# Performance work log

Measured on AMD Instinct MI355X. Metric: run time of the kernel, lower is better.

The kernel has to match this reference:

```python
import jax, jax.numpy as jnp
import numpy as np

NUM_CLASSES = 1000
N, C = 8192, 256

def setup_inputs() -> dict:
    key = jax.random.key(0)
    k1, k2, k3 = jax.random.split(key, 3)
    p = jax.random.normal(k1, (N, C), dtype=jnp.float32)
    z = jax.random.normal(k2, (N, C), dtype=jnp.float32)
    t = jax.random.uniform(k3, (N, NUM_CLASSES), dtype=jnp.float32, minval=1e-4, maxval=1.0)
    targets = t / jnp.sum(t, axis=1, keepdims=True)  # valid soft-label distribution
    return {"p": p, "z": z, "targets": targets}

def reference(p, z, targets):
    z = jax.lax.stop_gradient(z)  # z.detach()
    # F.normalize(dim=1), eps=1e-12
    p = p / jnp.maximum(jnp.linalg.norm(p, axis=1, keepdims=True), 1e-12)
    zn = z / jnp.maximum(jnp.linalg.norm(z, axis=1, keepdims=True), 1e-12)
    dot_product = -jnp.matmul(p, zn.T)  # [N, N]
    # entropy of soft targets, NaN rows (any exact-zero entry) zeroed
    prod = targets * jnp.log(targets)
    entr = -jnp.sum(prod, axis=1)
    entr = jnp.where(jnp.isnan(entr), 0.0, entr)
    norm_entr = entr / jnp.log(jnp.float32(NUM_CLASSES))
    r = 1.0 - norm_entr
    mask1 = jnp.outer(r, r)  # [N, N]
    # cosine similarity Gram of targets (torch cosine_similarity eps=1e-8)
    tnorm = jnp.linalg.norm(targets, axis=1)
    denom = jnp.maximum(tnorm[:, None] * tnorm[None, :], 1e-8)
    mask2 = jnp.matmul(targets, targets.T) / denom  # [N, N]
    n = dot_product.shape[0]
    mask_anchor_out = 1.0 - jnp.eye(n, dtype=dot_product.dtype)
    mask_combined = mask1 * mask2 * mask_anchor_out
    sel = dot_product * mask_combined
    # mean over nonzero entries (jit-safe: sum / count of nonzeros)
    nz = (sel != 0.0)
    return jnp.sum(sel) / jnp.sum(nz).astype(sel.dtype)
```

## Files before the change

### kernel.cpp

```cpp
#include <hip/hip_runtime.h>
#include <math.h>

#define NROWS 8192
#define CDIM 256
#define KDIM 1000
#define KPAD 1024

#define BC 128
#define BK 64
#define BI 8

typedef __attribute__((ext_vector_type(8))) short bf16x8;
typedef __attribute__((ext_vector_type(4))) float f32x4;
typedef _Float16 f16;
typedef __attribute__((ext_vector_type(4))) _Float16 f16x4;

__device__ __forceinline__ unsigned short f2bf(float x) {
  unsigned int u = __float_as_uint(x);
  u += 0x7fffu + ((u >> 16) & 1u);
  return (unsigned short)(u >> 16);
}
__device__ __forceinline__ float bf2f(unsigned short h) {
  return __uint_as_float(((unsigned int)h) << 16);
}

__device__ __forceinline__ void gl16(const void* g, void* l) {
  __builtin_amdgcn_global_load_lds(
      (const __attribute__((address_space(1))) unsigned int*)g,
      (__attribute__((address_space(3))) unsigned int*)l, 16, 0, 0);
}

__global__ __launch_bounds__(256, 4) void prep_kernel(
    const float* __restrict__ p, const float* __restrict__ z,
    const float* __restrict__ t,
    unsigned short* __restrict__ gAhi, unsigned short* __restrict__ gAlo,
    unsigned short* __restrict__ gBhi, unsigned short* __restrict__ gBlo,
    unsigned short* __restrict__ gUhi, unsigned short* __restrict__ gUlo,
    float* __restrict__ diag) {
  __shared__ float tbuf[8 * 1028];
  __shared__ float st_s[8], uu_s[8], sa_s[8], sb_s[8];
  __shared__ double r_s[8];
  const int tid = threadIdx.x;
  const int w = tid >> 6, lane = tid & 63;
  const int stripe = blockIdx.x;
  const int istep = stripe >> 2;
  const int qtr = stripe & 3;
  const int i0 = stripe * 8;

#pragma unroll
  for (int rr = 0; rr < 2; ++rr) {
    const int row = 2 * w + rr;
    const float* trow = t + (size_t)(i0 + row) * KDIM;
    float stt = 0.f, ent = 0.f, zfl = 0.f;
#pragma unroll
    for (int c = 0; c < 4; ++c) {
      const int k4 = c * 64 + lane;
      float4 v = make_float4(0.f, 0.f, 0.f, 0.f);
      if (k4 < 250) {
        v = *(const float4*)(trow + k4 * 4);
        const float vv[4] = {v.x, v.y, v.z, v.w};
#pragma unroll
        for (int q = 0; q < 4; ++q) {
          stt += vv[q] * vv[q];
          if (vv[q] > 0.f) ent += vv[q] * logf(vv[q]);
          else zfl = 1.f;
        }
      }
      *(float4*)&tbuf[row * 1028 + k4 * 4] = v;
    }
#pragma unroll
    for (int off = 32; off; off >>= 1) {
      stt += __shfl_xor(stt, off);
      ent += __shfl_xor(ent, off);
      zfl += __shfl_xor(zfl, off);
    }
    if (lane == 0) {
      const float tnorm = sqrtf(stt);
      st_s[row] = 1.f / tnorm;
      uu_s[row] = stt / (tnorm * tnorm);
      const float entr = (zfl > 0.f) ? 0.f : (-ent);
      r_s[row] = 1.0 - (double)entr / log(1000.0);
    }
  }
  __syncthreads();

#pragma unroll
  for (int it = 0; it < 4; ++it) {
    const int item = it * 256 + tid;
    const int kt8 = item >> 7;
    const int kf = (item >> 4) & 7;
    const int cl = item & 15;
    const int kcl = kf * 16 + cl;
    unsigned int hi[4], lo[4];
#pragma unroll
    for (int q = 0; q < 4; ++q) {
      const int r0 = 2 * q, r1 = r0 + 1;
      const float v0 = tbuf[r0 * 1028 + kt8 * 128 + kcl] * st_s[r0];
      const float v1 = tbuf[r1 * 1028 + kt8 * 128 + kcl] * st_s[r1];
      const unsigned short h0 = f2bf(v0), h1 = f2bf(v1);
      hi[q] = (unsigned int)h0 | ((unsigned int)h1 << 16);
      const unsigned short e0 = f2bf(v0 - bf2f(h0));
      const unsigned short e1 = f2bf(v1 - bf2f(h1));
      lo[q] = (unsigned int)e0 | ((unsigned int)e1 << 16);
    }
    const size_t off = ((size_t)(kt8 * 256 + istep)) * 8192
                       + (size_t)kf * 1024 + (size_t)(qtr * 16 + cl) * 16;
    *(uint4*)((char*)gUhi + off) = make_uint4(hi[0], hi[1], hi[2], hi[3]);
    *(uint4*)((char*)gUlo + off) = make_uint4(lo[0], lo[1], lo[2], lo[3]);
  }
  __syncthreads();

  float* ptile = tbuf;
  float* ztile = tbuf + 8 * 260;
#pragma unroll
  for (int rr = 0; rr < 2; ++rr) {
    const int row = 2 * w + rr;
    const float* prow = p + (size_t)(i0 + row) * CDIM;
    const float* zrow = z + (size_t)(i0 + row) * CDIM;
    const float4 pv = *(const float4*)(prow + lane * 4);
    const float4 zv = *(const float4*)(zrow + lane * 4);
    *(float4*)&ptile[row * 260 + lane * 4] = pv;
    *(float4*)&ztile[row * 260 + lane * 4] = zv;
    float sp = pv.x * pv.x + pv.y * pv.y + pv.z * pv.z + pv.w * pv.w;
    float sz = zv.x * zv.x + zv.y * zv.y + zv.z * zv.z + zv.w * zv.w;
    float spz = pv.x * zv.x + pv.y * zv.y + pv.z * zv.z + pv.w * zv.w;
#pragma unroll
    for (int off = 32; off; off >>= 1) {
      sp += __shfl_xor(sp, off);
      sz += __shfl_xor(sz, off);
      spz += __shfl_xor(spz, off);
    }
    if (lane == 0) {
      const double r = r_s[row];
      const float pnorm = sqrtf(sp), znorm = sqrtf(sz);
      const float sav = (float)(r / fmax((double)pnorm, 1e-12));
      const float sbv = (float)(r / fmax((double)znorm, 1e-12));
      sa_s[row] = sav; sb_s[row] = sbv;
      diag[i0 + row] = spz * sav * sbv * uu_s[row];
    }
  }
  __syncthreads();

  {
    const int cfg = tid >> 4;
    const int cl = tid & 15;
    const int crd = cfg * 16 + cl;
#pragma unroll 1
    for (int which = 0; which < 2; ++which) {
      const float* tile = which ? ztile : ptile;
      const float* ss = which ? sb_s : sa_s;
      unsigned short* ghi = which ? gBhi : gAhi;
      unsigned short* glo = which ? gBlo : gAlo;
      unsigned int hi[4], lo[4];
#pragma unroll
      for (int q = 0; q < 4; ++q) {
        const int r0 = 2 * q, r1 = r0 + 1;
        const float v0 = tile[r0 * 260 + crd] * ss[r0];
        const float v1 = tile[r1 * 260 + crd] * ss[r1];
        const unsigned short h0 = f2bf(v0), h1 = f2bf(v1);
        hi[q] = (unsigned int)h0 | ((unsigned int)h1 << 16);
        const unsigned short e0 = f2bf(v0 - bf2f(h0));
        const unsigned short e1 = f2bf(v1 - bf2f(h1));
        lo[q] = (unsigned int)e0 | ((unsigned int)e1 << 16);
      }
      const size_t off = ((size_t)((cfg >> 3) * 256 + istep)) * 8192
                         + (size_t)(cfg & 7) * 1024 + (size_t)(qtr * 16 + cl) * 16;
      *(uint4*)((char*)ghi + off) = make_uint4(hi[0], hi[1], hi[2], hi[3]);
      *(uint4*)((char*)glo + off) = make_uint4(lo[0], lo[1], lo[2], lo[3]);
    }
  }
}

__global__ __launch_bounds__(512, 1) void mfma_gemm_kernel(
    const unsigned short* __restrict__ gAhi, const unsigned short* __restrict__ gAlo,
    const unsigned short* __restrict__ gBhi, const unsigned short* __restrict__ gBlo,
    const unsigned short* __restrict__ gUhi, const unsigned short* __restrict__ gUlo,
    f16* __restrict__ part1, f16* __restrict__ part2, int steps) {
  __shared__ unsigned short lds[2][32768];
  const int tid = threadIdx.x;
  const int lane = tid & 63;
  const int wid = tid >> 6;
  const int wr = wid >> 1, wc = wid & 1;
  const int ct = blockIdx.x, kt = blockIdx.y, zc = blockIdx.z;
  const int istep0 = zc * steps;

  f32x4 acc1[2][8], acc2[2][8];
#pragma unroll
  for (int c = 0; c < 2; ++c)
#pragma unroll
    for (int k = 0; k < 8; ++k) {
      acc1[c][k] = (f32x4){0.f, 0.f, 0.f, 0.f};
      acc2[c][k] = (f32x4){0.f, 0.f, 0.f, 0.f};
    }

  const char* sA[4] = {(const char*)gAhi, (const char*)gAlo,
                       (const char*)gBhi, (const char*)gBlo};

  auto stage = [&](int buf, int s) {
    const size_t ab = ((size_t)(ct * 256 + istep0 + s)) * 8192 + (size_t)tid * 16;
    const size_t ub0 = ((size_t)((2 * kt) * 256 + istep0 + s)) * 8192 + (size_t)tid * 16;
    const size_t ub1 = ((size_t)((2 * kt + 1) * 256 + istep0 + s)) * 8192 + (size_t)tid * 16;
#pragma unroll
    for (int pl = 0; pl < 4; ++pl)
      gl16(sA[pl] + ab, &lds[buf][pl * 4096 + tid * 8]);
    gl16((const char*)gUhi + ub0, &lds[buf][16384 + tid * 8]);
    gl16((const char*)gUhi + ub1, &lds[buf][16384 + 4096 + tid * 8]);
    gl16((const char*)gUlo + ub0, &lds[buf][24576 + tid * 8]);
    gl16((const char*)gUlo + ub1, &lds[buf][24576 + 4096 + tid * 8]);
  };

  stage(0, 0);
  for (int s = 0; s < steps; ++s) {
    const int cur = s & 1;
    if (s + 1 < steps) {
      stage(cur ^ 1, s + 1);
      asm volatile("s_waitcnt vmcnt(8)" ::: "memory");
    } else {
      asm volatile("s_waitcnt vmcnt(0)" ::: "memory");
    }
    __builtin_amdgcn_s_barrier();
    asm volatile("" ::: "memory");

    bf16x8 ah[2], al[2], bh[2], bl[2];
#pragma unroll
    for (int c = 0; c < 2; ++c) {
      const int cf = wr * 2 + c;
      ah[c] = *(const bf16x8*)&lds[cur][0 * 4096 + (cf * 64 + lane) * 8];
      al[c] = *(const bf16x8*)&lds[cur][1 * 4096 + (cf * 64 + lane) * 8];
      bh[c] = *(const bf16x8*)&lds[cur][2 * 4096 + (cf * 64 + lane) * 8];
      bl[c] = *(const bf16x8*)&lds[cur][3 * 4096 + (cf * 64 + lane) * 8];
    }
    __builtin_amdgcn_s_setprio(1);
#pragma unroll
    for (int kh = 0; kh < 4; ++kh) {
      bf16x8 uh[2], ul[2];
#pragma unroll
      for (int k2 = 0; k2 < 2; ++k2) {
        const int kfg = wc * 8 + kh * 2 + k2;
        uh[k2] = *(const bf16x8*)&lds[cur][16384 + (kfg * 64 + lane) * 8];
        ul[k2] = *(const bf16x8*)&lds[cur][24576 + (kfg * 64 + lane) * 8];
      }
#pragma unroll
      for (int k2 = 0; k2 < 2; ++k2) {
        const int k = kh * 2 + k2;
#pragma unroll
        for (int c = 0; c < 2; ++c) {
          acc1[c][k] = __builtin_amdgcn_mfma_f32_16x16x32_bf16(ah[c], uh[k2], acc1[c][k], 0, 0, 0);
          acc1[c][k] = __builtin_amdgcn_mfma_f32_16x16x32_bf16(al[c], uh[k2], acc1[c][k], 0, 0, 0);
          acc1[c][k] = __builtin_amdgcn_mfma_f32_16x16x32_bf16(ah[c], ul[k2], acc1[c][k], 0, 0, 0);
          acc2[c][k] = __builtin_amdgcn_mfma_f32_16x16x32_bf16(bh[c], uh[k2], acc2[c][k], 0, 0, 0);
          acc2[c][k] = __builtin_amdgcn_mfma_f32_16x16x32_bf16(bl[c], uh[k2], acc2[c][k], 0, 0, 0);
          acc2[c][k] = __builtin_amdgcn_mfma_f32_16x16x32_bf16(bh[c], ul[k2], acc2[c][k], 0, 0, 0);
        }
      }
    }
    __builtin_amdgcn_s_setprio(0);
    __builtin_amdgcn_s_barrier();
  }

  f16* o1 = part1 + (size_t)zc * (CDIM * KPAD);
  f16* o2 = part2 + (size_t)zc * (CDIM * KPAD);
#pragma unroll
  for (int c = 0; c < 2; ++c)
#pragma unroll
    for (int k = 0; k < 8; ++k)
#pragma unroll
      for (int j = 0; j < 4; ++j) {
        const int cg = ct * 128 + (wr * 2 + c) * 16 + (lane >> 4) * 4 + j;
        const int kg = kt * 256 + (wc * 8 + k) * 16 + (lane & 15);
        o1[(size_t)cg * KPAD + kg] = (f16)acc1[c][k][j];
        o2[(size_t)cg * KPAD + kg] = (f16)acc2[c][k][j];
      }
}

__global__ __launch_bounds__(256) void reduce_h_kernel(
    const f16* __restrict__ part1, const f16* __restrict__ part2,
    double* __restrict__ bsum, int split) {
  const int tid = threadIdx.x;
  const size_t base = ((size_t)blockIdx.x * 256 + tid) * 4;
  double m1[4] = {0, 0, 0, 0}, m2[4] = {0, 0, 0, 0};
#pragma unroll 4
  for (int zz = 0; zz < split; ++zz) {
    const f16x4 a = *(const f16x4*)(part1 + (size_t)zz * (CDIM * KPAD) + base);
    const f16x4 b = *(const f16x4*)(part2 + (size_t)zz * (CDIM * KPAD) + base);
#pragma unroll
    for (int e = 0; e < 4; ++e) {
      m1[e] += (double)(float)a[e];
      m2[e] += (double)(float)b[e];
    }
  }
  double s = 0.0;
#pragma unroll
  for (int e = 0; e < 4; ++e) s += m1[e] * m2[e];
  __shared__ double red[256];
  red[tid] = s;
  __syncthreads();
  for (int off = 128; off; off >>= 1) {
    if (tid < off) red[tid] += red[tid + off];
    __syncthreads();
  }
  if (tid == 0) bsum[blockIdx.x] = red[0];
}

__global__ __launch_bounds__(256) void rowstats_kernel(
    const float* __restrict__ p, const float* __restrict__ z,
    const float* __restrict__ t,
    float* __restrict__ sa, float* __restrict__ sb,
    float* __restrict__ st, float* __restrict__ diag) {
  const int i = blockIdx.x;
  const int tid = threadIdx.x;
  const float pv = p[(size_t)i * CDIM + tid];
  const float zv = z[(size_t)i * CDIM + tid];
  float sp = pv * pv, sz = zv * zv, spz = pv * zv;
  float stt = 0.f, ent = 0.f, zfl = 0.f;
  const float* trow = t + (size_t)i * KDIM;
  for (int k = tid; k < KDIM; k += 256) {
    const float tv = trow[k];
    stt += tv * tv;
    if (tv > 0.f) ent += tv * logf(tv);
    else zfl = 1.f;
  }
#pragma unroll
  for (int off = 32; off; off >>= 1) {
    sp  += __shfl_down(sp, off);
    sz  += __shfl_down(sz, off);
    spz += __shfl_down(spz, off);
    stt += __shfl_down(stt, off);
    ent += __shfl_down(ent, off);
    zfl += __shfl_down(zfl, off);
  }
  __shared__ float wred[4][6];
  const int wid = tid >> 6, lane = tid & 63;
  if (lane == 0) {
    wred[wid][0] = sp;  wred[wid][1] = sz;  wred[wid][2] = spz;
    wred[wid][3] = stt; wred[wid][4] = ent; wred[wid][5] = zfl;
  }
  __syncthreads();
  if (tid == 0) {
    sp  = wred[0][0] + wred[1][0] + wred[2][0] + wred[3][0];
    sz  = wred[0][1] + wred[1][1] + wred[2][1] + wred[3][1];
    spz = wred[0][2] + wred[1][2] + wred[2][2] + wred[3][2];
    stt = wred[0][3] + wred[1][3] + wred[2][3] + wred[3][3];
    ent = wred[0][4] + wred[1][4] + wred[2][4] + wred[3][4];
    zfl = wred[0][5] + wred[1][5] + wred[2][5] + wred[3][5];
    const float pnorm = sqrtf(sp);
    const float znorm = sqrtf(sz);
    const float tnorm = sqrtf(stt);
    const float entr = (zfl > 0.f) ? 0.f : (-ent);
    const double r = 1.0 - (double)entr / log(1000.0);
    const float sav = (float)(r / fmax((double)pnorm, 1e-12));
    const float sbv = (float)(r / fmax((double)znorm, 1e-12));
    const float stv = 1.f / tnorm;
    const float uu = stt / (tnorm * tnorm);
    sa[i] = sav; sb[i] = sbv; st[i] = stv;
    diag[i] = spz * sav * sbv * uu;
  }
}

__global__ __launch_bounds__(256) void fp32_gemm_kernel(
    const float* __restrict__ p, const float* __restrict__ z,
    const float* __restrict__ t,
    const float* __restrict__ sa, const float* __restrict__ sb,
    const float* __restrict__ st,
    float* __restrict__ part1, float* __restrict__ part2, int ichunk) {
  __shared__ float As[BI][BC];
  __shared__ float Bs[BI][BC];
  __shared__ float Us[BI][BK];
  const int tid = threadIdx.x;
  const int c0 = blockIdx.x * BC;
  const int k0 = blockIdx.y * BK;
  const int i0 = blockIdx.z * ichunk;
  float acc1[8][4] = {{0.f}};
  float acc2[8][4] = {{0.f}};
  const int tc = tid & 15;
  const int tk = tid >> 4;
  const int lrow = tid >> 5;
  const int lcolA = (tid & 31) * 4;
  const int lcolU = (tid & 31) * 2;
  for (int ib = 0; ib < ichunk; ib += BI) {
    const int i = i0 + ib + lrow;
    const float sav = sa[i], sbv = sb[i], stv = st[i];
    const float4 pv = *(const float4*)(p + (size_t)i * CDIM + c0 + lcolA);
    const float4 zv = *(const float4*)(z + (size_t)i * CDIM + c0 + lcolA);
    const int kk = k0 + lcolU;
    const float u0 = (kk     < KDIM) ? t[(size_t)i * KDIM + kk]     * stv : 0.f;
    const float u1 = (kk + 1 < KDIM) ? t[(size_t)i * KDIM + kk + 1] * stv : 0.f;
    __syncthreads();
    *(float4*)&As[lrow][lcolA] = make_float4(pv.x * sav, pv.y * sav, pv.z * sav, pv.w * sav);
    *(float4*)&Bs[lrow][lcolA] = make_float4(zv.x * sbv, zv.y * sbv, zv.z * sbv, zv.w * sbv);
    Us[lrow][lcolU] = u0;
    Us[lrow][lcolU + 1] = u1;
    __syncthreads();
#pragma unroll
    for (int ii = 0; ii < BI; ++ii) {
      const float4 a0 = *(const float4*)&As[ii][tc * 8];
      const float4 a1 = *(const float4*)&As[ii][tc * 8 + 4];
      const float4 b0 = *(const float4*)&Bs[ii][tc * 8];
      const float4 b1 = *(const float4*)&Bs[ii][tc * 8 + 4];
      const float4 u  = *(const float4*)&Us[ii][tk * 4];
      const float a[8] = {a0.x, a0.y, a0.z, a0.w, a1.x, a1.y, a1.z, a1.w};
      const float b[8] = {b0.x, b0.y, b0.z, b0.w, b1.x, b1.y, b1.z, b1.w};
      const float uv[4] = {u.x, u.y, u.z, u.w};
#pragma unroll
      for (int m = 0; m < 8; ++m)
#pragma unroll
        for (int n = 0; n < 4; ++n) {
          acc1[m][n] = fmaf(a[m], uv[n], acc1[m][n]);
          acc2[m][n] = fmaf(b[m], uv[n], acc2[m][n]);
        }
    }
  }
  float* o1 = part1 + (size_t)blockIdx.z * (CDIM * KPAD);
  float* o2 = part2 + (size_t)blockIdx.z * (CDIM * KPAD);
#pragma unroll
  for (int m = 0; m < 8; ++m) {
    const int c = c0 + tc * 8 + m;
    const int k = k0 + tk * 4;
    *(float4*)&o1[(size_t)c * KPAD + k] = *(const float4*)acc1[m];
    *(float4*)&o2[(size_t)c * KPAD + k] = *(const float4*)acc2[m];
  }
}

__global__ __launch_bounds__(256) void reduce_kernel(
    const float* __restrict__ part1, const float* __restrict__ part2,
    double* __restrict__ bsum, int split) {
  const int tid = threadIdx.x;
  double s = 0.0;
  for (int r = 0; r < 4; ++r) {
    const size_t idx = (size_t)blockIdx.x * 1024 + (size_t)r * 256 + tid;
    double m1 = 0.0, m2 = 0.0;
    for (int zz = 0; zz < split; ++zz) {
      m1 += (double)part1[(size_t)zz * (CDIM * KPAD) + idx];
      m2 += (double)part2[(size_t)zz * (CDIM * KPAD) + idx];
    }
    s += m1 * m2;
  }
  __shared__ double red[256];
  red[tid] = s;
  __syncthreads();
  for (int off = 128; off; off >>= 1) {
    if (tid < off) red[tid] += red[tid + off];
    __syncthreads();
  }
  if (tid == 0) bsum[blockIdx.x] = red[0];
}

__global__ __launch_bounds__(256) void final_kernel(
    const double* __restrict__ bsum, const float* __restrict__ diag,
    float* __restrict__ out, int nb) {
  const int tid = threadIdx.x;
  double s = 0.0;
  for (int i = tid; i < nb; i += 256) s += bsum[i];
  double d = 0.0;
  for (int i = tid; i < NROWS; i += 256) d += (double)diag[i];
  __shared__ double red[256];
  red[tid] = s;
  __syncthreads();
  for (int off = 128; off; off >>= 1) {
    if (tid < off) red[tid] += red[tid + off];
    __syncthreads();
  }
  double s_all = red[0];
  __syncthreads();
  red[tid] = d;
  __syncthreads();
  for (int off = 128; off; off >>= 1) {
    if (tid < off) red[tid] += red[tid + off];
    __syncthreads();
  }
  if (tid == 0) {
    const double s_diag = red[0];
    const double sel_sum = -(s_all - s_diag);
    const double cnt = (double)NROWS * (double)NROWS - (double)NROWS;
    out[0] = (float)(sel_sum / cnt);
  }
}

extern "C" void kernel_launch(void* const* d_in, const int* in_sizes, int n_in,
                              void* d_out, int out_size, void* d_ws, size_t ws_size,
                              hipStream_t stream) {
  const float* p = (const float*)d_in[0];
  const float* z = (const float*)d_in[1];
  const float* t = (const float*)d_in[2];
  float* out = (float*)d_out;
  char* ws = (char*)d_ws;

  float* sa = (float*)ws;
  float* sb = sa + NROWS;
  float* st = sb + NROWS;
  float* diag = st + NROWS;
  const size_t statsB = (size_t)4 * NROWS * sizeof(float);

  const size_t planeA = (size_t)2 * 256 * 8 * 1024;
  const size_t planeU = (size_t)8 * 256 * 8 * 1024;
  const size_t chunkH = (size_t)CDIM * KPAD * 2;
  const size_t chunkF = (size_t)CDIM * KPAD * 4;

  int split = 32;
  while (split > 4 &&
         statsB + 4 * planeA + 2 * planeU + (size_t)split * 2 * chunkH + 8192 > ws_size)
    split >>= 1;
  const bool use_mfma =
      statsB + 4 * planeA + 2 * planeU + (size_t)split * 2 * chunkH + 8192 <= ws_size;

  if (use_mfma) {
    char* base = ws + statsB;
    unsigned short* gAhi = (unsigned short*)(base);
    unsigned short* gAlo = (unsigned short*)(base + planeA);
    unsigned short* gBhi = (unsigned short*)(base + 2 * planeA);
    unsigned short* gBlo = (unsigned short*)(base + 3 * planeA);
    unsigned short* gUhi = (unsigned short*)(base + 4 * planeA);
    unsigned short* gUlo = (unsigned short*)(base + 4 * planeA + planeU);
    f16* part1 = (f16*)(base + 4 * planeA + 2 * planeU);
    f16* part2 = part1 + (size_t)split * (CDIM * KPAD);
    double* bsum = (double*)(part2 + (size_t)split * (CDIM * KPAD));
    const int steps = (NROWS / split) / 32;

    hipLaunchKernelGGL(prep_kernel, dim3(1024), dim3(256), 0, stream,
                       p, z, t, gAhi, gAlo, gBhi, gBlo, gUhi, gUlo, diag);
    hipLaunchKernelGGL(mfma_gemm_kernel, dim3(2, 4, split), dim3(512), 0, stream,
                       gAhi, gAlo, gBhi, gBlo, gUhi, gUlo, part1, part2, steps);
    hipLaunchKernelGGL(reduce_h_kernel, dim3(256), dim3(256), 0, stream,
                       part1, part2, bsum, split);
    hipLaunchKernelGGL(final_kernel, dim3(1), dim3(256), 0, stream,
                       bsum, diag, out, 256);
  } else {
    int osplit = 16;
    while (osplit > 1 &&
           statsB + (size_t)osplit * chunkF * 2 + 8192 > ws_size)
      osplit >>= 1;
    float* part1 = (float*)(ws + statsB);
    float* part2 = part1 + (size_t)osplit * (CDIM * KPAD);
    double* bsum = (double*)(part2 + (size_t)osplit * (CDIM * KPAD));
    hipLaunchKernelGGL(rowstats_kernel, dim3(NROWS), dim3(256), 0, stream,
                       p, z, t, sa, sb, st, diag);
    hipLaunchKernelGGL(fp32_gemm_kernel, dim3(CDIM / BC, KPAD / BK, osplit),
                       dim3(256), 0, stream,
                       p, z, t, sa, sb, st, part1, part2, NROWS / osplit);
    hipLaunchKernelGGL(reduce_kernel, dim3(256), dim3(256), 0, stream,
                       part1, part2, bsum, osplit);
    hipLaunchKernelGGL(final_kernel, dim3(1), dim3(256), 0, stream,
                       bsum, diag, out, 256);
  }
}
```

Before: 70.43 us.

## Triple-buffer A tiles and drop trailing barrier in MFMA GEMM pipeline

Splits the LDS staging into separate A and U buffers, using a 3-deep ring for the A/B planes and a 2-deep ring for U. Next-step loads are now issued after the barrier, which lets the per-iteration trailing barrier go. A tiles are prefetched two steps ahead to hide more global-load latency. LDS use grows from 128KB to 160KB. The buffer-reuse ordering has to be right for the single remaining barrier to be race-free.

```diff
diff --git a/kernel.cpp b/kernel.cpp
--- a/kernel.cpp
+++ b/kernel.cpp
@@ -176,7 +176,7 @@
     const unsigned short* __restrict__ gBhi, const unsigned short* __restrict__ gBlo,
     const unsigned short* __restrict__ gUhi, const unsigned short* __restrict__ gUlo,
     f16* __restrict__ part1, f16* __restrict__ part2, int steps) {
-  __shared__ unsigned short lds[2][32768];
+  __shared__ unsigned short lds[81920];
   const int tid = threadIdx.x;
   const int lane = tid & 63;
   const int wid = tid >> 6;
@@ -196,39 +196,49 @@
   const char* sA[4] = {(const char*)gAhi, (const char*)gAlo,
                        (const char*)gBhi, (const char*)gBlo};
 
-  auto stage = [&](int buf, int s) {
+  auto stageA = [&](int buf, int s) {
     const size_t ab = ((size_t)(ct * 256 + istep0 + s)) * 8192 + (size_t)tid * 16;
+#pragma unroll
+    for (int pl = 0; pl < 4; ++pl)
+      gl16(sA[pl] + ab, &lds[buf * 16384 + pl * 4096 + tid * 8]);
+  };
+  auto stageU = [&](int buf, int s) {
     const size_t ub0 = ((size_t)((2 * kt) * 256 + istep0 + s)) * 8192 + (size_t)tid * 16;
     const size_t ub1 = ((size_t)((2 * kt + 1) * 256 + istep0 + s)) * 8192 + (size_t)tid * 16;
-#pragma unroll
-    for (int pl = 0; pl < 4; ++pl)
-      gl16(sA[pl] + ab, &lds[buf][pl * 4096 + tid * 8]);
-    gl16((const char*)gUhi + ub0, &lds[buf][16384 + tid * 8]);
-    gl16((const char*)gUhi + ub1, &lds[buf][16384 + 4096 + tid * 8]);
-    gl16((const char*)gUlo + ub0, &lds[buf][24576 + tid * 8]);
-    gl16((const char*)gUlo + ub1, &lds[buf][24576 + 4096 + tid * 8]);
+    unsigned short* base = &lds[49152 + buf * 16384];
+    gl16((const char*)gUhi + ub0, base + tid * 8);
+    gl16((const char*)gUhi + ub1, base + 4096 + tid * 8);
+    gl16((const char*)gUlo + ub0, base + 8192 + tid * 8);
+    gl16((const char*)gUlo + ub1, base + 8192 + 4096 + tid * 8);
   };
 
-  stage(0, 0);
+  stageA(0, 0);
+  stageU(0, 0);
+  if (steps > 1) stageA(1, 1);
+
   for (int s = 0; s < steps; ++s) {
-    const int cur = s & 1;
+    const int ca = s % 3, cu = s & 1;
     if (s + 1 < steps) {
-      stage(cur ^ 1, s + 1);
-      asm volatile("s_waitcnt vmcnt(8)" ::: "memory");
+      asm volatile("s_waitcnt vmcnt(4)" ::: "memory");
     } else {
       asm volatile("s_waitcnt vmcnt(0)" ::: "memory");
     }
     __builtin_amdgcn_s_barrier();
     asm volatile("" ::: "memory");
+    if (s + 1 < steps) stageU(cu ^ 1, s + 1);
+    if (s + 2 < steps) stageA((s + 2) % 3, s + 2);
+
+    const unsigned short* Ab = &lds[ca * 16384];
+    const unsigned short* Ub = &lds[49152 + cu * 16384];
 
     bf16x8 ah[2], al[2], bh[2], bl[2];
 #pragma unroll
     for (int c = 0; c < 2; ++c) {
       const int cf = wr * 2 + c;
-      ah[c] = *(const bf16x8*)&lds[cur][0 * 4096 + (cf * 64 + lane) * 8];
-      al[c] = *(const bf16x8*)&lds[cur][1 * 4096 + (cf * 64 + lane) * 8];
-      bh[c] = *(const bf16x8*)&lds[cur][2 * 4096 + (cf * 64 + lane) * 8];
-      bl[c] = *(const bf16x8*)&lds[cur][3 * 4096 + (cf * 64 + lane) * 8];
+      ah[c] = *(const bf16x8*)&Ab[0 * 4096 + (cf * 64 + lane) * 8];
+      al[c] = *(const bf16x8*)&Ab[1 * 4096 + (cf * 64 + lane) * 8];
+      bh[c] = *(const bf16x8*)&Ab[2 * 4096 + (cf * 64 + lane) * 8];
+      bl[c] = *(const bf16x8*)&Ab[3 * 4096 + (cf * 64 + lane) * 8];
     }
     __builtin_amdgcn_s_setprio(1);
 #pragma unroll
@@ -237,8 +247,8 @@
 #pragma unroll
       for (int k2 = 0; k2 < 2; ++k2) {
         const int kfg = wc * 8 + kh * 2 + k2;
-        uh[k2] = *(const bf16x8*)&lds[cur][16384 + (kfg * 64 + lane) * 8];
-        ul[k2] = *(const bf16x8*)&lds[cur][24576 + (kfg * 64 + lane) * 8];
+        uh[k2] = *(const bf16x8*)&Ub[(kfg * 64 + lane) * 8];
+        ul[k2] = *(const bf16x8*)&Ub[8192 + (kfg * 64 + lane) * 8];
       }
 #pragma unroll
       for (int k2 = 0; k2 < 2; ++k2) {
@@ -255,7 +265,6 @@
       }
     }
     __builtin_amdgcn_s_setprio(0);
-    __builtin_amdgcn_s_barrier();
   }
 
   f16* o1 = part1 + (size_t)zc * (CDIM * KPAD);
```

New measurement: 69.30 us. About the same (-1.6%).
